# Optimization experiments

Hardware: AMD Instinct MI355X
Metric: run time of the kernel (lower is better)

The kernel has to match this reference:

```python
import jax, jax.numpy as jnp
import numpy as np

B, S, D, H = 2, 2048, 1024, 16
HD = D // H
SCALE = HD ** -0.5
NEG = -1e30


def setup_inputs() -> dict:
    key = jax.random.key(0)
    ks = jax.random.split(key, 10)
    w = lambda k: jax.random.normal(k, (D, D), dtype=jnp.float32) * 0.02
    b = lambda k: jax.random.normal(k, (D,), dtype=jnp.float32) * 0.01
    hidden_states = jax.random.normal(ks[0], (B, S, D), dtype=jnp.float32)
    document_ids = jnp.sort(jax.random.randint(ks[1], (S,), 0, 16))
    return {
        'hidden_states': hidden_states,
        'wq': w(ks[2]), 'bq': b(ks[3]),
        'wk': w(ks[4]), 'bk': b(ks[5]),
        'wv': w(ks[6]), 'bv': b(ks[7]),
        'wo': w(ks[8]), 'bo': b(ks[9]),
        'document_ids': document_ids,
    }


def reference(hidden_states, wq, bq, wk, bk, wv, bv, wo, bo, document_ids):
    # projections (nn.Linear: x @ W.T + b)
    q = (hidden_states @ wq.T + bq).reshape(B, S, H, HD)
    k = (hidden_states @ wk.T + bk).reshape(B, S, H, HD)
    v = (hidden_states @ wv.T + bv).reshape(B, S, H, HD)
    # document-block mask: attend only within same document
    mask = document_ids[:, None] == document_ids[None, :]  # [S, S]
    scores = jnp.einsum('bqhd,bkhd->bhqk', q, k) * SCALE
    scores = jnp.where(mask[None, None], scores, NEG)
    attn = jax.nn.softmax(scores, axis=-1)
    out = jnp.einsum('bhqk,bkhd->bqhd', attn, v).reshape(B, S, D)
    return out @ wo.T + bo
```

## Files before the change

kernel.cpp:

```cpp
#include <hip/hip_runtime.h>
#include <hip/hip_bf16.h>
#include <math.h>

#define B 2
#define S 2048
#define D 1024
#define H 16
#define HD 64
#define SCALE 0.125f
#define NEGBIG -1e30f

#define NE 4194304
#define NW 1048576
#define NE8 524288
#define NW8 131072

typedef _Float16 f16;
typedef _Float16 f16x8 __attribute__((ext_vector_type(8)));
typedef _Float16 f16x4 __attribute__((ext_vector_type(4)));
typedef float f32x4  __attribute__((ext_vector_type(4)));

__device__ __forceinline__ void gl_lds16(const void* g, void* l) {
    __builtin_amdgcn_global_load_lds(
        (const __attribute__((address_space(1))) unsigned int*)g,
        (__attribute__((address_space(3))) unsigned int*)l, 16, 0, 0);
}

__device__ __forceinline__ void wave_lds_fence() {
    __builtin_amdgcn_wave_barrier();
    __builtin_amdgcn_s_waitcnt(0xC07F);
    __builtin_amdgcn_wave_barrier();
}

__global__ __launch_bounds__(256) void prep_k(
    const float4* __restrict__ hs,
    const float4* __restrict__ wq, const float4* __restrict__ wk,
    const float4* __restrict__ wv, const float4* __restrict__ wo,
    const int* __restrict__ doc,
    f16x8* __restrict__ xh, f16x8* __restrict__ wqkv, f16x8* __restrict__ woh,
    int* __restrict__ dstart, int* __restrict__ dend)
{
    int i = blockIdx.x * blockDim.x + threadIdx.x;
    if (i < NE8 + 4 * NW8) {
        const float4* src;
        f16x8* dst;
        if (i < NE8) { src = hs + 2 * (size_t)i; dst = xh + i; }
        else {
            int j = i - NE8;
            int id = j / NW8, jj = j - id * NW8;
            src = ((id == 0) ? wq : (id == 1) ? wk : (id == 2) ? wv : wo) + 2 * (size_t)jj;
            dst = (id < 3) ? (wqkv + (size_t)id * NW8 + jj) : (woh + jj);
        }
        float4 a = src[0], b = src[1];
        f16x8 h;
        h[0] = (f16)a.x; h[1] = (f16)a.y; h[2] = (f16)a.z; h[3] = (f16)a.w;
        h[4] = (f16)b.x; h[5] = (f16)b.y; h[6] = (f16)b.z; h[7] = (f16)b.w;
        *dst = h;
    } else {
        int s = i - (NE8 + 4 * NW8);
        if (s < S) {
            int v = doc[s];
            int lo = 0, hi = S;
            while (lo < hi) { int mid = (lo + hi) >> 1; if (doc[mid] < v) lo = mid + 1; else hi = mid; }
            dstart[s] = lo;
            lo = 0; hi = S;
            while (lo < hi) { int mid = (lo + hi) >> 1; if (doc[mid] <= v) lo = mid + 1; else hi = mid; }
            dend[s] = lo;
        }
    }
}

__global__ __launch_bounds__(512, 2) void qkv_mfma_k(
    const f16* __restrict__ xh, const f16* __restrict__ wqkv,
    const float* __restrict__ bq, const float* __restrict__ bk,
    const float* __restrict__ bv,
    f16* __restrict__ Qh, f16* __restrict__ Kh, f16* __restrict__ Vth)
{
    __shared__ union {
        struct { f16 At[2][256 * 64]; f16 Bt[2][256 * 64]; } s;
        f16 tr[64 * 264];
    } lds;

    const int which = blockIdx.z;
    const f16* Bg = wqkv + (size_t)which * D * D;

    const int tid = threadIdx.x;
    const int w = tid >> 6, ln = tid & 63;
    const int wm = (w & 1) * 128, wn = (w >> 1) * 64;
    const int lc = ln & 15, quad = ln >> 4;
    const int m0 = blockIdx.y * 256, n0 = blockIdx.x * 256;

    size_t aoff[4], boff[4];
    int ldst[4];
    #pragma unroll
    for (int i = 0; i < 4; i++) {
        int r = w * 32 + i * 8 + (ln >> 3);
        int o = (ln & 7) ^ (r & 7);
        aoff[i] = (size_t)(m0 + r) * 1024 + o * 8;
        boff[i] = (size_t)(n0 + r) * 1024 + o * 8;
        ldst[i] = (w * 32 + i * 8) * 64;
    }

    f32x4 acc[8][4];
    #pragma unroll
    for (int i = 0; i < 8; i++)
        #pragma unroll
        for (int j = 0; j < 4; j++) acc[i][j] = (f32x4){0.f, 0.f, 0.f, 0.f};

    #define STAGE(buf, k0) { \
        f16* Ad_ = lds.s.At[buf]; f16* Bd_ = lds.s.Bt[buf]; \
        _Pragma("unroll") \
        for (int i_ = 0; i_ < 4; i_++) gl_lds16(xh + aoff[i_] + (k0), Ad_ + ldst[i_]); \
        _Pragma("unroll") \
        for (int i_ = 0; i_ < 4; i_++) gl_lds16(Bg + boff[i_] + (k0), Bd_ + ldst[i_]); }

    STAGE(0, 0)
    STAGE(1, 64)
    asm volatile("s_waitcnt vmcnt(8)");
    __builtin_amdgcn_sched_barrier(0);
    __builtin_amdgcn_s_barrier();
    __builtin_amdgcn_sched_barrier(0);

    for (int kt = 0; kt < 16; ++kt) {
        const int cur = kt & 1;
        const f16* Acur = lds.s.At[cur];
        const f16* Bcur = lds.s.Bt[cur];

        f16x8 bf[4][2];
        #pragma unroll
        for (int t = 0; t < 4; t++) {
            int bn = wn + t * 16 + lc;
            #pragma unroll
            for (int ks = 0; ks < 2; ks++)
                bf[t][ks] = *(const f16x8*)&Bcur[bn * 64 + (((ks * 4 + quad) ^ (bn & 7)) * 8)];
        }

        #pragma unroll
        for (int q = 0; q < 4; ++q) {
            f16x8 af[2][2];
            #pragma unroll
            for (int t = 0; t < 2; t++) {
                int am = wm + (q * 2 + t) * 16 + lc;
                #pragma unroll
                for (int ks = 0; ks < 2; ks++)
                    af[t][ks] = *(const f16x8*)&Acur[am * 64 + (((ks * 4 + quad) ^ (am & 7)) * 8)];
            }
            __builtin_amdgcn_s_setprio(1);
            #pragma unroll
            for (int ks = 0; ks < 2; ks++)
                #pragma unroll
                for (int mt = 0; mt < 2; mt++)
                    #pragma unroll
                    for (int nt = 0; nt < 4; nt++)
                        acc[q * 2 + mt][nt] = __builtin_amdgcn_mfma_f32_16x16x32_f16(
                            af[mt][ks], bf[nt][ks], acc[q * 2 + mt][nt], 0, 0, 0);
            __builtin_amdgcn_s_setprio(0);
        }

        if (kt == 15) break;

        __builtin_amdgcn_s_barrier();
        __builtin_amdgcn_sched_barrier(0);
        if (kt + 2 < 16) {
            STAGE(cur, (kt + 2) * 64)
            asm volatile("s_waitcnt vmcnt(8)");
        } else {
            asm volatile("s_waitcnt vmcnt(0)");
        }
        __builtin_amdgcn_sched_barrier(0);
        __builtin_amdgcn_s_barrier();
        __builtin_amdgcn_sched_barrier(0);
    }
    #undef STAGE

    if (which < 2) {
        const float* bias = (which == 0) ? bq : bk;
        f16* dst = (which == 0) ? Qh : Kh;
        #pragma unroll
        for (int nt = 0; nt < 4; nt++) {
            int col = n0 + wn + nt * 16 + lc;
            float bias_v = bias[col];
            int h = col >> 6, hd = col & 63;
            #pragma unroll
            for (int mt = 0; mt < 8; mt++) {
                #pragma unroll
                for (int r = 0; r < 4; r++) {
                    int m = m0 + wm + mt * 16 + quad * 4 + r;
                    int bbm = m >> 11, s = m & (S - 1);
                    float val = acc[mt][nt][r] + bias_v;
                    if (which == 0) val *= SCALE;
                    size_t idx = (((size_t)(bbm * H + h) * S) + s) * HD + hd;
                    dst[idx] = (f16)val;
                }
            }
        }
    } else {
        const int bb = m0 >> 11;
        const int sbase = m0 & (S - 1);
        __syncthreads();
        #pragma unroll
        for (int pass = 0; pass < 4; pass++) {
            if ((w >> 1) == pass) {
                #pragma unroll
                for (int nt = 0; nt < 4; nt++) {
                    int colp = nt * 16 + lc;
                    float bvv = bv[n0 + pass * 64 + colp];
                    #pragma unroll
                    for (int mt = 0; mt < 8; mt++) {
                        f16x4 v;
                        #pragma unroll
                        for (int r = 0; r < 4; r++) v[r] = (f16)(acc[mt][nt][r] + bvv);
                        *(f16x4*)&lds.tr[colp * 264 + wm + mt * 16 + quad * 4] = v;
                    }
                }
            }
            __syncthreads();
            #pragma unroll
            for (int p2 = 0; p2 < 4; p2++) {
                int chunk = tid + p2 * 512;
                int colp = chunk >> 5;
                int oct = chunk & 31;
                f16x8 v = *(const f16x8*)&lds.tr[colp * 264 + oct * 8];
                int vcol = n0 + pass * 64 + colp;
                int h = vcol >> 6, hd = vcol & 63;
                size_t idx = (((size_t)(bb * H + h) * HD) + hd) * S + sbase + oct * 8;
                *(f16x8*)(Vth + idx) = v;
            }
            __syncthreads();
        }
    }
}

__global__ __launch_bounds__(256) void out_mfma_k(
    const f16* __restrict__ oh, const f16* __restrict__ wh,
    const float* __restrict__ bias, float* __restrict__ Y)
{
    __shared__ f16 Ah[128 * 64], Bh[64 * 64];
    const int tid = threadIdx.x;
    const int w = tid >> 6, ln = tid & 63;
    const int wm = (w & 1) * 64, wn = (w >> 1) * 32;
    const int lc = ln & 15, quad = ln >> 4;
    const int m0 = blockIdx.y * 128, n0 = blockIdx.x * 64;

    f32x4 acc[4][2];
    #pragma unroll
    for (int i = 0; i < 4; i++)
        #pragma unroll
        for (int j = 0; j < 2; j++) acc[i][j] = (f32x4){0.f, 0.f, 0.f, 0.f};

    for (int k0 = 0; k0 < 1024; k0 += 64) {
        #pragma unroll
        for (int i = 0; i < 4; i++) {
            int rl = w * 32 + i * 8 + (ln >> 3);
            int oc = (ln & 7) ^ (rl & 7);
            gl_lds16(oh + (size_t)(m0 + rl) * 1024 + k0 + oc * 8, Ah + (w * 32 + i * 8) * 64);
        }
        #pragma unroll
        for (int i = 0; i < 2; i++) {
            int rl = w * 16 + i * 8 + (ln >> 3);
            int oc = (ln & 7) ^ (rl & 7);
            gl_lds16(wh + (size_t)(n0 + rl) * 1024 + k0 + oc * 8, Bh + (w * 16 + i * 8) * 64);
        }
        __syncthreads();

        #pragma unroll
        for (int ks = 0; ks < 2; ks++) {
            f16x8 ah[4], bh[2];
            #pragma unroll
            for (int t = 0; t < 4; t++) {
                int am = wm + t * 16 + lc;
                ah[t] = *(const f16x8*)&Ah[am * 64 + (((ks * 4 + quad) ^ (am & 7)) * 8)];
            }
            #pragma unroll
            for (int t = 0; t < 2; t++) {
                int bn = wn + t * 16 + lc;
                bh[t] = *(const f16x8*)&Bh[bn * 64 + (((ks * 4 + quad) ^ (bn & 7)) * 8)];
            }
            #pragma unroll
            for (int mt = 0; mt < 4; mt++)
                #pragma unroll
                for (int nt = 0; nt < 2; nt++)
                    acc[mt][nt] = __builtin_amdgcn_mfma_f32_16x16x32_f16(ah[mt], bh[nt], acc[mt][nt], 0, 0, 0);
        }
        __syncthreads();
    }

    #pragma unroll
    for (int nt = 0; nt < 2; nt++) {
        int col = n0 + wn + nt * 16 + lc;
        float bv_ = bias[col];
        #pragma unroll
        for (int mt = 0; mt < 4; mt++) {
            #pragma unroll
            for (int r = 0; r < 4; r++) {
                int m = m0 + wm + mt * 16 + quad * 4 + r;
                Y[(size_t)m * D + col] = acc[mt][nt][r] + bv_;
            }
        }
    }
}

__device__ __forceinline__ void load_kfrag(
    const f16* __restrict__ Kh, size_t bh, int j0, int lc, int quad, f16x8 kf[4][2])
{
    #pragma unroll
    for (int t = 0; t < 4; t++) {
        size_t krow = (bh + j0 + t * 16 + lc) * HD;
        #pragma unroll
        for (int ks = 0; ks < 2; ks++)
            kf[t][ks] = *(const f16x8*)(Kh + krow + ks * 32 + quad * 8);
    }
}

__global__ __launch_bounds__(256) void attn4_k(
    const f16* __restrict__ Qh, const f16* __restrict__ Kh,
    const f16* __restrict__ Vth,
    const int* __restrict__ dstart, const int* __restrict__ dend,
    f16* __restrict__ Ohi)
{
    const int qt = blockIdx.x, h = blockIdx.y, b = blockIdx.z;
    const int tid = threadIdx.x;
    const int w = tid >> 6, ln = tid & 63;
    const int lc = ln & 15, quad = ln >> 4;
    const int q0 = qt * 64 + w * 16;
    const size_t bh  = ((size_t)b * H + h) * S;
    const size_t bhv = ((size_t)b * H + h) * HD;

    __shared__ float Ps[4][2][16 * 65];

    int row_st[4], row_en[4];
    #pragma unroll
    for (int r = 0; r < 4; r++) {
        row_st[r] = dstart[q0 + quad * 4 + r];
        row_en[r] = dend[q0 + quad * 4 + r];
    }
    const int kstart = dstart[q0] & ~63;
    const int kend   = dend[q0 + 15];

    const size_t qrow = bh + q0 + lc;
    f16x8 qf[2];
    #pragma unroll
    for (int ks = 0; ks < 2; ks++)
        qf[ks] = *(const f16x8*)(Qh + qrow * HD + ks * 32 + quad * 8);

    f32x4 o[4];
    #pragma unroll
    for (int nt = 0; nt < 4; nt++) o[nt] = (f32x4){0.f, 0.f, 0.f, 0.f};
    f32x4 m_i = (f32x4){NEGBIG, NEGBIG, NEGBIG, NEGBIG};
    f32x4 l_i = (f32x4){0.f, 0.f, 0.f, 0.f};

    f16x8 kf[4][2], kf2[4][2];
    load_kfrag(Kh, bh, kstart, lc, quad, kf);

    int it = 0;
    for (int j0 = kstart; j0 < kend; j0 += 64, it ^= 1) {
        float* ps = &Ps[w][it][0];
        const bool more = (j0 + 64) < kend;
        if (more) load_kfrag(Kh, bh, j0 + 64, lc, quad, kf2);

        f32x4 sc[4];
        #pragma unroll
        for (int t = 0; t < 4; t++) {
            f32x4 a = (f32x4){0.f, 0.f, 0.f, 0.f};
            #pragma unroll
            for (int ks = 0; ks < 2; ks++)
                a = __builtin_amdgcn_mfma_f32_16x16x32_f16(qf[ks], kf[t][ks], a, 0, 0, 0);
            int key = j0 + t * 16 + lc;
            #pragma unroll
            for (int r = 0; r < 4; r++) {
                bool valid = (key >= row_st[r]) && (key < row_en[r]);
                sc[t][r] = valid ? a[r] : NEGBIG;
            }
        }

        f32x4 mx = sc[0];
        #pragma unroll
        for (int t = 1; t < 4; t++)
            #pragma unroll
            for (int r = 0; r < 4; r++) mx[r] = fmaxf(mx[r], sc[t][r]);
        #pragma unroll
        for (int off = 1; off <= 8; off <<= 1)
            #pragma unroll
            for (int r = 0; r < 4; r++) mx[r] = fmaxf(mx[r], __shfl_xor(mx[r], off, 64));

        f32x4 m_new, alpha;
        #pragma unroll
        for (int r = 0; r < 4; r++) {
            m_new[r] = fmaxf(m_i[r], mx[r]);
            alpha[r] = __expf(m_i[r] - m_new[r]);
        }

        f32x4 psum = (f32x4){0.f, 0.f, 0.f, 0.f};
        f32x4 pv[4];
        #pragma unroll
        for (int t = 0; t < 4; t++) {
            #pragma unroll
            for (int r = 0; r < 4; r++) {
                float p = __expf(sc[t][r] - m_new[r]);
                p = (sc[t][r] < -5e29f) ? 0.f : p;
                pv[t][r] = p;
                psum[r] += p;
            }
        }
        #pragma unroll
        for (int off = 1; off <= 8; off <<= 1)
            #pragma unroll
            for (int r = 0; r < 4; r++) psum[r] += __shfl_xor(psum[r], off, 64);

        #pragma unroll
        for (int r = 0; r < 4; r++) {
            l_i[r] = l_i[r] * alpha[r] + psum[r];
            m_i[r] = m_new[r];
        }
        #pragma unroll
        for (int nt = 0; nt < 4; nt++)
            #pragma unroll
            for (int r = 0; r < 4; r++) o[nt][r] *= alpha[r];

        f16x8 vh[2][4];
        #pragma unroll
        for (int ks = 0; ks < 2; ks++) {
            int gp = ks * 4 + quad;
            #pragma unroll
            for (int nt = 0; nt < 4; nt++) {
                int dim = nt * 16 + lc;
                vh[ks][nt] = *(const f16x8*)(Vth + (bhv + dim) * S + j0 + gp * 8);
            }
        }

        #pragma unroll
        for (int t = 0; t < 4; t++) {
            int g = 2 * t + (lc >> 3);
            #pragma unroll
            for (int r = 0; r < 4; r++) {
                int q = quad * 4 + r;
                ps[q * 65 + ((g ^ (q & 7)) * 8) + (lc & 7)] = pv[t][r];
            }
        }

        wave_lds_fence();

        #pragma unroll
        for (int ks = 0; ks < 2; ks++) {
            int gp = ks * 4 + quad;
            const float* prow = &ps[lc * 65 + ((gp ^ (lc & 7)) * 8)];
            f16x8 ph;
            #pragma unroll
            for (int j = 0; j < 8; j++) ph[j] = (f16)prow[j];
            #pragma unroll
            for (int nt = 0; nt < 4; nt++)
                o[nt] = __builtin_amdgcn_mfma_f32_16x16x32_f16(ph, vh[ks][nt], o[nt], 0, 0, 0);
        }

        if (more) {
            #pragma unroll
            for (int t = 0; t < 4; t++)
                #pragma unroll
                for (int ks = 0; ks < 2; ks++) kf[t][ks] = kf2[t][ks];
        }
    }

    f32x4 inv;
    #pragma unroll
    for (int r = 0; r < 4; r++) inv[r] = 1.f / l_i[r];
    #pragma unroll
    for (int nt = 0; nt < 4; nt++) {
        int dim = nt * 16 + lc;
        #pragma unroll
        for (int r = 0; r < 4; r++) {
            int q = q0 + quad * 4 + r;
            float val = o[nt][r] * inv[r];
            size_t idx = ((size_t)(b * S + q)) * D + h * 64 + dim;
            Ohi[idx] = (f16)val;
        }
    }
}

extern "C" void kernel_launch(void* const* d_in, const int* in_sizes, int n_in,
                              void* d_out, int out_size, void* d_ws, size_t ws_size,
                              hipStream_t stream) {
    const float* hs = (const float*)d_in[0];
    const float* wq = (const float*)d_in[1];
    const float* bq = (const float*)d_in[2];
    const float* wk = (const float*)d_in[3];
    const float* bk = (const float*)d_in[4];
    const float* wv = (const float*)d_in[5];
    const float* bv = (const float*)d_in[6];
    const float* wo = (const float*)d_in[7];
    const float* bo = (const float*)d_in[8];
    const int*  doc = (const int*)d_in[9];
    float* out = (float*)d_out;

    f16* xh   = (f16*)d_ws;
    f16* Qhb  = xh + NE;
    f16* Khb  = Qhb + NE;
    f16* Vth  = Khb + NE;
    f16* wqkv = Vth + NE;
    f16* woh  = wqkv + 3 * (size_t)NW;
    int* dstart = (int*)(woh + NW);
    int* dend = dstart + S;

    prep_k<<<(NE8 + 4 * NW8 + S + 255) / 256, 256, 0, stream>>>(
        (const float4*)hs, (const float4*)wq, (const float4*)wk,
        (const float4*)wv, (const float4*)wo, doc,
        (f16x8*)xh, (f16x8*)wqkv, (f16x8*)woh, dstart, dend);

    qkv_mfma_k<<<dim3(D / 256, (B * S) / 256, 3), 512, 0, stream>>>(
        xh, wqkv, bq, bk, bv, Qhb, Khb, Vth);
    attn4_k<<<dim3(S / 64, H, B), 256, 0, stream>>>(
        Qhb, Khb, Vth, dstart, dend, xh);
    out_mfma_k<<<dim3(D / 64, (B * S) / 128), 256, 0, stream>>>(xh, woh, bo, out);
}
```

Before: 185.5 us.

## Double-buffer output projection GEMM with async global-to-LDS prefetch

Converts the output-projection MFMA kernel to a two-stage LDS ring. The next K tile is issued via global_load_lds while the current tile is computed, with explicit vmcnt waits and raw barriers replacing __syncthreads. Load address offsets are hoisted out of the loop, and MFMA issue is wrapped in setprio. This doubles LDS use for the kernel, which may reduce occupancy, and it depends on the hand-counted vmcnt values being correct.

```diff
diff --git a/kernel.cpp b/kernel.cpp
--- a/kernel.cpp
+++ b/kernel.cpp
@@ -235,33 +235,54 @@
     const f16* __restrict__ oh, const f16* __restrict__ wh,
     const float* __restrict__ bias, float* __restrict__ Y)
 {
-    __shared__ f16 Ah[128 * 64], Bh[64 * 64];
+    __shared__ f16 Ah[2][128 * 64];
+    __shared__ f16 Bh[2][64 * 64];
     const int tid = threadIdx.x;
     const int w = tid >> 6, ln = tid & 63;
     const int wm = (w & 1) * 64, wn = (w >> 1) * 32;
     const int lc = ln & 15, quad = ln >> 4;
     const int m0 = blockIdx.y * 128, n0 = blockIdx.x * 64;
 
+    size_t aoff[4], boff[2];
+    int lA[4], lB[2];
+    #pragma unroll
+    for (int i = 0; i < 4; i++) {
+        int rl = w * 32 + i * 8 + (ln >> 3);
+        int oc = (ln & 7) ^ (rl & 7);
+        aoff[i] = (size_t)(m0 + rl) * 1024 + oc * 8;
+        lA[i] = (w * 32 + i * 8) * 64;
+    }
+    #pragma unroll
+    for (int i = 0; i < 2; i++) {
+        int rl = w * 16 + i * 8 + (ln >> 3);
+        int oc = (ln & 7) ^ (rl & 7);
+        boff[i] = (size_t)(n0 + rl) * 1024 + oc * 8;
+        lB[i] = (w * 16 + i * 8) * 64;
+    }
+
     f32x4 acc[4][2];
     #pragma unroll
     for (int i = 0; i < 4; i++)
         #pragma unroll
         for (int j = 0; j < 2; j++) acc[i][j] = (f32x4){0.f, 0.f, 0.f, 0.f};
 
-    for (int k0 = 0; k0 < 1024; k0 += 64) {
-        #pragma unroll
-        for (int i = 0; i < 4; i++) {
-            int rl = w * 32 + i * 8 + (ln >> 3);
-            int oc = (ln & 7) ^ (rl & 7);
-            gl_lds16(oh + (size_t)(m0 + rl) * 1024 + k0 + oc * 8, Ah + (w * 32 + i * 8) * 64);
-        }
-        #pragma unroll
-        for (int i = 0; i < 2; i++) {
-            int rl = w * 16 + i * 8 + (ln >> 3);
-            int oc = (ln & 7) ^ (rl & 7);
-            gl_lds16(wh + (size_t)(n0 + rl) * 1024 + k0 + oc * 8, Bh + (w * 16 + i * 8) * 64);
-        }
-        __syncthreads();
+    #define OSTAGE(buf, k0) { \
+        _Pragma("unroll") \
+        for (int i_ = 0; i_ < 4; i_++) gl_lds16(oh + aoff[i_] + (k0), Ah[buf] + lA[i_]); \
+        _Pragma("unroll") \
+        for (int i_ = 0; i_ < 2; i_++) gl_lds16(wh + boff[i_] + (k0), Bh[buf] + lB[i_]); }
+
+    OSTAGE(0, 0)
+    OSTAGE(1, 64)
+    asm volatile("s_waitcnt vmcnt(6)");
+    __builtin_amdgcn_sched_barrier(0);
+    __builtin_amdgcn_s_barrier();
+    __builtin_amdgcn_sched_barrier(0);
+
+    for (int kt = 0; kt < 16; ++kt) {
+        const int cur = kt & 1;
+        const f16* Ac = Ah[cur];
+        const f16* Bc = Bh[cur];
 
         #pragma unroll
         for (int ks = 0; ks < 2; ks++) {
@@ -269,21 +290,37 @@
             #pragma unroll
             for (int t = 0; t < 4; t++) {
                 int am = wm + t * 16 + lc;
-                ah[t] = *(const f16x8*)&Ah[am * 64 + (((ks * 4 + quad) ^ (am & 7)) * 8)];
+                ah[t] = *(const f16x8*)&Ac[am * 64 + (((ks * 4 + quad) ^ (am & 7)) * 8)];
             }
             #pragma unroll
             for (int t = 0; t < 2; t++) {
                 int bn = wn + t * 16 + lc;
-                bh[t] = *(const f16x8*)&Bh[bn * 64 + (((ks * 4 + quad) ^ (bn & 7)) * 8)];
-            }
+                bh[t] = *(const f16x8*)&Bc[bn * 64 + (((ks * 4 + quad) ^ (bn & 7)) * 8)];
+            }
+            __builtin_amdgcn_s_setprio(1);
             #pragma unroll
             for (int mt = 0; mt < 4; mt++)
                 #pragma unroll
                 for (int nt = 0; nt < 2; nt++)
                     acc[mt][nt] = __builtin_amdgcn_mfma_f32_16x16x32_f16(ah[mt], bh[nt], acc[mt][nt], 0, 0, 0);
-        }
-        __syncthreads();
-    }
+            __builtin_amdgcn_s_setprio(0);
+        }
+
+        if (kt == 15) break;
+
+        __builtin_amdgcn_s_barrier();
+        __builtin_amdgcn_sched_barrier(0);
+        if (kt + 2 < 16) {
+            OSTAGE(cur, (kt + 2) * 64)
+            asm volatile("s_waitcnt vmcnt(6)");
+        } else {
+            asm volatile("s_waitcnt vmcnt(0)");
+        }
+        __builtin_amdgcn_sched_barrier(0);
+        __builtin_amdgcn_s_barrier();
+        __builtin_amdgcn_sched_barrier(0);
+    }
+    #undef OSTAGE
 
     #pragma unroll
     for (int nt = 0; nt < 2; nt++) {
```

New measurement: 186.2 us. About the same (+0.4%).
